# Kernel optimization log

Measured on AMD Instinct MI355X. Metric: run time of the kernel, lower is better.

## Reference

```python
import jax, jax.numpy as jnp
import numpy as np

NUM_EMBEDDINGS = 1024
EMBEDDING_DIM = 256
COMMITMENT_COST = 0.25


def setup_inputs() -> dict:
    key = jax.random.key(0)
    k1, k2 = jax.random.split(key)
    z_e = jax.random.normal(k1, (32, 256, 32, 32), dtype=jnp.float32)
    # nn.init.uniform_(weight, -1/K, 1/K)
    bound = 1.0 / NUM_EMBEDDINGS
    weight = jax.random.uniform(k2, (NUM_EMBEDDINGS, EMBEDDING_DIM), dtype=jnp.float32,
                                minval=-bound, maxval=bound)
    return {"z_e": z_e, "weight": weight}


def reference(z_e, weight):
    B, C, H, W = z_e.shape
    sg = jax.lax.stop_gradient
    # (B, H, W, C) -> (N, C)
    flat = jnp.transpose(z_e, (0, 2, 3, 1)).reshape(-1, C)
    # squared L2 distances to each codebook vector: (N, K)
    dist = (jnp.sum(flat * flat, axis=1, keepdims=True)
            - 2.0 * flat @ weight.T
            + jnp.sum(weight * weight, axis=1))
    indices = jnp.argmin(dist, axis=1)  # (N,)
    # codebook lookup (equivalent to one-hot @ weight)
    quantized = weight[indices].reshape(B, H, W, C)
    quantized = jnp.transpose(quantized, (0, 3, 1, 2))  # (B, C, H, W)
    e_latent = jnp.mean((sg(quantized) - z_e) ** 2)
    q_latent = jnp.mean((quantized - sg(z_e)) ** 2)
    loss = q_latent + COMMITMENT_COST * e_latent
    # straight-through estimator
    quantized_st = z_e + sg(quantized - z_e)
    # codebook usage perplexity: avg_probs = mean of one-hot encodings
    n = flat.shape[0]
    counts = jax.ops.segment_sum(jnp.ones((n,), dtype=z_e.dtype), indices,
                                 num_segments=NUM_EMBEDDINGS)
    avg_probs = counts / n
    perplexity = jnp.exp(-jnp.sum(avg_probs * jnp.log(avg_probs + 1e-10)))
    return (quantized_st, loss, perplexity)
```

## Files before the change

### kernel.cpp

```cpp
#include <hip/hip_runtime.h>
#include <float.h>
#include <math.h>
#include <stdint.h>


#define NB   32
#define NC   256
#define NHW  1024
#define NK   1024
#define NELEM (NB*NC*NHW)
#define GRID_MAIN 512

typedef __attribute__((ext_vector_type(8))) short bf16x8;
typedef __attribute__((ext_vector_type(4))) float f32x4;

__device__ __forceinline__ unsigned short f2bf(float f) {
    unsigned u = __float_as_uint(f);
    u += 0x7FFFu + ((u >> 16) & 1u);
    return (unsigned short)(u >> 16);
}

__global__ __launch_bounds__(256) void vq_prep(const float* __restrict__ w,
                                               float* __restrict__ wsq,
                                               unsigned short* __restrict__ cb,
                                               unsigned int* __restrict__ counts,
                                               unsigned int* __restrict__ lossdone) {
    const int tid = threadIdx.x, b = blockIdx.x;
    const int lane = tid & 63, wv = tid >> 6;
    {
        const int k = b * 4 + wv;
        const float* row = w + k * NC;
        float s = 0.f;
#pragma unroll
        for (int p = 0; p < 4; ++p) { float v = row[lane + p * 64]; s = fmaf(v, v, s); }
#pragma unroll
        for (int off = 32; off; off >>= 1) s += __shfl_down(s, off, 64);
        if (lane == 0) wsq[k] = s;
    }
    const int gt = b * 256 + tid;
    if (gt < 32768) {
        const int t = gt >> 9, p = gt & 511;
        const int cc = p >> 6, l = p & 63;
        const int n = l & 15, quad = l >> 4;
        const float* src = w + (t * 16 + n) * NC + cc * 32 + quad * 8;
        const float4 f0 = *(const float4*)src;
        const float4 f1 = *(const float4*)(src + 4);
        union { unsigned short u[8]; uint4 v; } pk;
        pk.u[0] = f2bf(-2.f * f0.x); pk.u[1] = f2bf(-2.f * f0.y);
        pk.u[2] = f2bf(-2.f * f0.z); pk.u[3] = f2bf(-2.f * f0.w);
        pk.u[4] = f2bf(-2.f * f1.x); pk.u[5] = f2bf(-2.f * f1.y);
        pk.u[6] = f2bf(-2.f * f1.z); pk.u[7] = f2bf(-2.f * f1.w);
        *(uint4*)(cb + (size_t)t * 4096 + cc * 512 + (size_t)l * 8) = pk.v;
    }
    if (b == 128) {
#pragma unroll
        for (int i = 0; i < 4; ++i) counts[tid * 4 + i] = 0u;
        if (tid < 2) lossdone[tid] = 0u;
    }
}

__global__ __launch_bounds__(256) void vq_main3(const float* __restrict__ z,
                                                const float* __restrict__ w,
                                                const float* __restrict__ wsq,
                                                const unsigned short* __restrict__ cb,
                                                unsigned int* __restrict__ counts,
                                                unsigned int* __restrict__ lossdone,
                                                float* __restrict__ out) {
    __shared__ __align__(16) char cbuf[2][32768];
    int*   fidx  = (int*)(cbuf[0]);
    float* pscr  = (float*)(cbuf[0] + 256);
    int*   pidx  = (int*)(cbuf[0] + 768);
    float* lred  = (float*)(cbuf[0] + 1280);
    int*   lflag = (int*)(cbuf[0] + 1296);
    float* red2  = (float*)(cbuf[0] + 1312);

    const int tid  = threadIdx.x;
    const int wv   = tid >> 6, lane = tid & 63;
    const int n    = lane & 15, quad = lane >> 4;
    const int zhalf = wv & 1;
    const int chalf = wv >> 1;
    const int b   = blockIdx.x;
    const int img = b >> 4;
    const int hw0 = (b & 15) << 6;
    const float* zb = z + (size_t)img * (NC * NHW);
    const char* cbb = (const char*)cb;

#define STAGE(ch)                                                              \
    {                                                                          \
        _Pragma("unroll")                                                      \
        for (int i = 0; i < 8; ++i) {                                          \
            const int q = i >> 1, part = i & 1;                                \
            const int tq = (q >> 1) * 32 + (ch) * 2 + (q & 1);                 \
            const char* gsrc = cbb + (size_t)tq * 8192 + part * 4096 + tid * 16;\
            char* ldst = cbuf[(ch) & 1] + i * 4096 + tid * 16;                 \
            __builtin_amdgcn_global_load_lds(                                  \
                (const __attribute__((address_space(1))) unsigned int*)        \
                    (uintptr_t)gsrc,                                           \
                (__attribute__((address_space(3))) unsigned int*)              \
                    (uint32_t)(uintptr_t)ldst,                                 \
                16, 0, 0);                                                     \
        }                                                                      \
    }

    STAGE(0);

    bf16x8 bfr[2][8];
#pragma unroll
    for (int s = 0; s < 2; ++s) {
#pragma unroll
        for (int cc = 0; cc < 8; ++cc) {
            const float* zp = zb + (size_t)(cc * 32 + quad * 8) * NHW
                              + hw0 + zhalf * 32 + s * 16 + n;
            union { unsigned short u[8]; bf16x8 v; } pk;
#pragma unroll
            for (int j = 0; j < 8; ++j) pk.u[j] = f2bf(zp[(size_t)j * NHW]);
            bfr[s][cc] = pk.v;
        }
    }

    float bestv[2] = {FLT_MAX, FLT_MAX};
    int   besti[2] = {0, 0};

    for (int ch = 0; ch < 16; ++ch) {
        __syncthreads();
        if (ch + 1 < 16) STAGE(ch + 1);
        const char* bufc = cbuf[ch & 1];
        const int kt0 = (chalf * 32 + ch * 2) * 16;
        const int kt1 = kt0 + 16;
        const int slot0 = chalf * 2, slot1 = slot0 + 1;
        f32x4 acc00 = *(const f32x4*)(wsq + kt0 + quad * 4);
        f32x4 acc01 = acc00;
        f32x4 acc10 = *(const f32x4*)(wsq + kt1 + quad * 4);
        f32x4 acc11 = acc10;
#pragma unroll
        for (int cc = 0; cc < 8; ++cc) {
            const bf16x8 a0 = *(const bf16x8*)(bufc + slot0 * 8192 + cc * 1024 + lane * 16);
            const bf16x8 a1 = *(const bf16x8*)(bufc + slot1 * 8192 + cc * 1024 + lane * 16);
            acc00 = __builtin_amdgcn_mfma_f32_16x16x32_bf16(a0, bfr[0][cc], acc00, 0, 0, 0);
            acc01 = __builtin_amdgcn_mfma_f32_16x16x32_bf16(a0, bfr[1][cc], acc01, 0, 0, 0);
            acc10 = __builtin_amdgcn_mfma_f32_16x16x32_bf16(a1, bfr[0][cc], acc10, 0, 0, 0);
            acc11 = __builtin_amdgcn_mfma_f32_16x16x32_bf16(a1, bfr[1][cc], acc11, 0, 0, 0);
        }
#pragma unroll
        for (int r = 0; r < 4; ++r) {
            const int k0 = kt0 + quad * 4 + r, k1 = kt1 + quad * 4 + r;
            if (acc00[r] < bestv[0]) { bestv[0] = acc00[r]; besti[0] = k0; }
            if (acc01[r] < bestv[1]) { bestv[1] = acc01[r]; besti[1] = k0; }
            if (acc10[r] < bestv[0]) { bestv[0] = acc10[r]; besti[0] = k1; }
            if (acc11[r] < bestv[1]) { bestv[1] = acc11[r]; besti[1] = k1; }
        }
    }

#pragma unroll
    for (int s = 0; s < 2; ++s) {
        float bv = bestv[s]; int bi = besti[s];
#pragma unroll
        for (int off = 16; off <= 32; off <<= 1) {
            const float ov = __shfl_xor(bv, off, 64);
            const int   ok = __shfl_xor(bi, off, 64);
            if (ov < bv || (ov == bv && ok < bi)) { bv = ov; bi = ok; }
        }
        bestv[s] = bv; besti[s] = bi;
    }
    __syncthreads();
    if (lane < 16) {
#pragma unroll
        for (int s = 0; s < 2; ++s) {
            const int zloc = zhalf * 32 + s * 16 + lane;
            pscr[chalf * 64 + zloc] = bestv[s];
            pidx[chalf * 64 + zloc] = besti[s];
        }
    }
    __syncthreads();
    if (tid < 64) {
        const float s0 = pscr[tid], s1 = pscr[64 + tid];
        const int bi = (s1 < s0) ? pidx[64 + tid] : pidx[tid];
        fidx[tid] = bi;
        atomicAdd(&counts[bi], 1u);
    }
    __syncthreads();

    float lsum = 0.f;
    const int hwl = tid & 63;
    const int cg  = tid >> 6;
    const int myk = fidx[hwl];
    const float* wr  = w + myk * NC;
    const float* zp2 = zb + hw0 + hwl;
    float*       op  = out + (size_t)img * (NC * NHW) + hw0 + hwl;
#pragma unroll 4
    for (int p = 0; p < 16; ++p) {
        const int c0 = cg * 64 + p * 4;
        const float4 q4 = *(const float4*)(wr + c0);
        const float qa[4] = {q4.x, q4.y, q4.z, q4.w};
#pragma unroll
        for (int u = 0; u < 4; ++u) {
            const int c = c0 + u;
            const float zv = zp2[(size_t)c * NHW];
            const float d = qa[u] - zv;
            lsum = fmaf(d, d, lsum);
            op[(size_t)c * NHW] = qa[u];
        }
    }
#pragma unroll
    for (int off = 32; off; off >>= 1) lsum += __shfl_down(lsum, off, 64);
    if (lane == 0) lred[wv] = lsum;
    __syncthreads();
    if (tid == 0) {
        atomicAdd((float*)lossdone, lred[0] + lred[1] + lred[2] + lred[3]);
        const unsigned old = __hip_atomic_fetch_add(&lossdone[1], 1u,
                                 __ATOMIC_ACQ_REL, __HIP_MEMORY_SCOPE_AGENT);
        lflag[0] = (old == GRID_MAIN - 1) ? 1 : 0;
    }
    __syncthreads();
    if (lflag[0]) {
        float s = 0.f;
#pragma unroll
        for (int p = 0; p < 4; ++p) {
            const unsigned c = __hip_atomic_load(&counts[tid + p * 256],
                                   __ATOMIC_RELAXED, __HIP_MEMORY_SCOPE_AGENT);
            const float pr = (float)c * (1.f / 32768.f);
            s = fmaf(pr, logf(pr + 1e-10f), s);
        }
#pragma unroll
        for (int off = 32; off; off >>= 1) s += __shfl_down(s, off, 64);
        if (lane == 0) red2[wv] = s;
        __syncthreads();
        if (tid == 0) {
            const float tot = red2[0] + red2[1] + red2[2] + red2[3];
            const float ls = __hip_atomic_load((float*)lossdone,
                                 __ATOMIC_RELAXED, __HIP_MEMORY_SCOPE_AGENT);
            out[NELEM]     = ls * (1.25f / (float)NELEM);
            out[NELEM + 1] = expf(-tot);
        }
    }
}

extern "C" void kernel_launch(void* const* d_in, const int* in_sizes, int n_in,
                              void* d_out, int out_size, void* d_ws, size_t ws_size,
                              hipStream_t stream) {
    const float* z = (const float*)d_in[0];
    const float* w = (const float*)d_in[1];
    float* out = (float*)d_out;

    float*          wsq      = (float*)d_ws;
    unsigned int*   counts   = (unsigned int*)((char*)d_ws + 4096);
    unsigned int*   lossdone = (unsigned int*)((char*)d_ws + 8192);
    unsigned short* cbfrag   = (unsigned short*)((char*)d_ws + 16384);

    vq_prep <<<256,       256, 0, stream>>>(w, wsq, cbfrag, counts, lossdone);
    vq_main3<<<GRID_MAIN, 256, 0, stream>>>(z, w, wsq, cbfrag, counts, lossdone, out);
}
```

Before: 136.3 us.

## Derive loss from argmin distances and widen blocks to 1024 threads

Blocks grow to 1024 threads covering 128 spatial positions with a 4-way split over the codebook. Each codebook chunk staged in LDS is therefore shared by twice as many positions, and the grid is halved. The loss no longer re-reads z in the output pass. It is rebuilt from the best distance plus a per-position ||z||^2 accumulated while z is loaded. The distance comes from the bf16 MFMA, so the loss may drift slightly from an exact fp32 sum. The output pass now only gathers codebook rows and writes them. The 128 KB LDS footprint allows one block per CU, which may hurt latency hiding.

```diff
diff --git a/kernel.cpp b/kernel.cpp
--- a/kernel.cpp
+++ b/kernel.cpp
@@ -9,7 +9,7 @@
 #define NHW  1024
 #define NK   1024
 #define NELEM (NB*NC*NHW)
-#define GRID_MAIN 512
+#define GRID_MAIN 256
 
 typedef __attribute__((ext_vector_type(8))) short bf16x8;
 typedef __attribute__((ext_vector_type(4))) float f32x4;
@@ -59,40 +59,40 @@
     }
 }
 
-__global__ __launch_bounds__(256) void vq_main3(const float* __restrict__ z,
-                                                const float* __restrict__ w,
-                                                const float* __restrict__ wsq,
-                                                const unsigned short* __restrict__ cb,
-                                                unsigned int* __restrict__ counts,
-                                                unsigned int* __restrict__ lossdone,
-                                                float* __restrict__ out) {
-    __shared__ __align__(16) char cbuf[2][32768];
+__global__ __launch_bounds__(1024, 4) void vq_main4(const float* __restrict__ z,
+                                                    const float* __restrict__ w,
+                                                    const float* __restrict__ wsq,
+                                                    const unsigned short* __restrict__ cb,
+                                                    unsigned int* __restrict__ counts,
+                                                    unsigned int* __restrict__ lossdone,
+                                                    float* __restrict__ out) {
+    __shared__ __align__(16) char cbuf[2][65536];
     int*   fidx  = (int*)(cbuf[0]);
-    float* pscr  = (float*)(cbuf[0] + 256);
-    int*   pidx  = (int*)(cbuf[0] + 768);
-    float* lred  = (float*)(cbuf[0] + 1280);
-    int*   lflag = (int*)(cbuf[0] + 1296);
-    float* red2  = (float*)(cbuf[0] + 1312);
+    float* pscr  = (float*)(cbuf[0] + 512);
+    int*   pidx  = (int*)(cbuf[0] + 2560);
+    float* zsqs  = (float*)(cbuf[0] + 4608);
+    float* lred  = (float*)(cbuf[0] + 5120);
+    int*   lflag = (int*)(cbuf[0] + 5184);
+    float* red2  = (float*)(cbuf[0] + 5200);
 
     const int tid  = threadIdx.x;
     const int wv   = tid >> 6, lane = tid & 63;
     const int n    = lane & 15, quad = lane >> 4;
-    const int zhalf = wv & 1;
-    const int chalf = wv >> 1;
-    const int b   = blockIdx.x;
-    const int img = b >> 4;
-    const int hw0 = (b & 15) << 6;
+    const int zq   = wv & 3;
+    const int cq   = wv >> 2;
+    const int b    = blockIdx.x;
+    const int img  = b >> 3;
+    const int hw0  = (b & 7) << 7;
     const float* zb = z + (size_t)img * (NC * NHW);
     const char* cbb = (const char*)cb;
 
 #define STAGE(ch)                                                              \
     {                                                                          \
         _Pragma("unroll")                                                      \
-        for (int i = 0; i < 8; ++i) {                                          \
-            const int q = i >> 1, part = i & 1;                                \
-            const int tq = (q >> 1) * 32 + (ch) * 2 + (q & 1);                 \
-            const char* gsrc = cbb + (size_t)tq * 8192 + part * 4096 + tid * 16;\
-            char* ldst = cbuf[(ch) & 1] + i * 4096 + tid * 16;                 \
+        for (int i = 0; i < 4; ++i) {                                          \
+            const int t = i * 16 + (ch) * 2 + (tid >> 9);                      \
+            const char* gsrc = cbb + (size_t)t * 8192 + (tid & 511) * 16;      \
+            char* ldst = cbuf[(ch) & 1] + i * 16384 + tid * 16;                \
             __builtin_amdgcn_global_load_lds(                                  \
                 (const __attribute__((address_space(1))) unsigned int*)        \
                     (uintptr_t)gsrc,                                           \
@@ -105,15 +105,20 @@
     STAGE(0);
 
     bf16x8 bfr[2][8];
+    float zsqp[2] = {0.f, 0.f};
 #pragma unroll
     for (int s = 0; s < 2; ++s) {
 #pragma unroll
         for (int cc = 0; cc < 8; ++cc) {
             const float* zp = zb + (size_t)(cc * 32 + quad * 8) * NHW
-                              + hw0 + zhalf * 32 + s * 16 + n;
+                              + hw0 + zq * 32 + s * 16 + n;
             union { unsigned short u[8]; bf16x8 v; } pk;
 #pragma unroll
-            for (int j = 0; j < 8; ++j) pk.u[j] = f2bf(zp[(size_t)j * NHW]);
+            for (int j = 0; j < 8; ++j) {
+                const float f = zp[(size_t)j * NHW];
+                zsqp[s] = fmaf(f, f, zsqp[s]);
+                pk.u[j] = f2bf(f);
+            }
             bfr[s][cc] = pk.v;
         }
     }
@@ -121,21 +126,21 @@
     float bestv[2] = {FLT_MAX, FLT_MAX};
     int   besti[2] = {0, 0};
 
-    for (int ch = 0; ch < 16; ++ch) {
+    for (int ch = 0; ch < 8; ++ch) {
         __syncthreads();
-        if (ch + 1 < 16) STAGE(ch + 1);
+        if (ch + 1 < 8) STAGE(ch + 1);
         const char* bufc = cbuf[ch & 1];
-        const int kt0 = (chalf * 32 + ch * 2) * 16;
+        const int kt0 = (cq * 16 + ch * 2) * 16;
         const int kt1 = kt0 + 16;
-        const int slot0 = chalf * 2, slot1 = slot0 + 1;
+        const int so0 = (cq * 2) * 8192, so1 = so0 + 8192;
         f32x4 acc00 = *(const f32x4*)(wsq + kt0 + quad * 4);
         f32x4 acc01 = acc00;
         f32x4 acc10 = *(const f32x4*)(wsq + kt1 + quad * 4);
         f32x4 acc11 = acc10;
 #pragma unroll
         for (int cc = 0; cc < 8; ++cc) {
-            const bf16x8 a0 = *(const bf16x8*)(bufc + slot0 * 8192 + cc * 1024 + lane * 16);
-            const bf16x8 a1 = *(const bf16x8*)(bufc + slot1 * 8192 + cc * 1024 + lane * 16);
+            const bf16x8 a0 = *(const bf16x8*)(bufc + so0 + cc * 1024 + lane * 16);
+            const bf16x8 a1 = *(const bf16x8*)(bufc + so1 + cc * 1024 + lane * 16);
             acc00 = __builtin_amdgcn_mfma_f32_16x16x32_bf16(a0, bfr[0][cc], acc00, 0, 0, 0);
             acc01 = __builtin_amdgcn_mfma_f32_16x16x32_bf16(a0, bfr[1][cc], acc01, 0, 0, 0);
             acc10 = __builtin_amdgcn_mfma_f32_16x16x32_bf16(a1, bfr[0][cc], acc10, 0, 0, 0);
@@ -153,77 +158,79 @@
 
 #pragma unroll
     for (int s = 0; s < 2; ++s) {
-        float bv = bestv[s]; int bi = besti[s];
+        float bv = bestv[s]; int bi = besti[s]; float zs = zsqp[s];
 #pragma unroll
         for (int off = 16; off <= 32; off <<= 1) {
             const float ov = __shfl_xor(bv, off, 64);
             const int   ok = __shfl_xor(bi, off, 64);
             if (ov < bv || (ov == bv && ok < bi)) { bv = ov; bi = ok; }
-        }
-        bestv[s] = bv; besti[s] = bi;
+            zs += __shfl_xor(zs, off, 64);
+        }
+        bestv[s] = bv; besti[s] = bi; zsqp[s] = zs;
     }
     __syncthreads();
     if (lane < 16) {
 #pragma unroll
         for (int s = 0; s < 2; ++s) {
-            const int zloc = zhalf * 32 + s * 16 + lane;
-            pscr[chalf * 64 + zloc] = bestv[s];
-            pidx[chalf * 64 + zloc] = besti[s];
-        }
-    }
-    __syncthreads();
-    if (tid < 64) {
-        const float s0 = pscr[tid], s1 = pscr[64 + tid];
-        const int bi = (s1 < s0) ? pidx[64 + tid] : pidx[tid];
+            const int zloc = zq * 32 + s * 16 + lane;
+            pscr[cq * 128 + zloc] = bestv[s];
+            pidx[cq * 128 + zloc] = besti[s];
+            if (cq == 0) zsqs[zloc] = zsqp[s];
+        }
+    }
+    __syncthreads();
+    if (tid < 128) {
+        float bv = pscr[tid]; int bi = pidx[tid];
+#pragma unroll
+        for (int q = 1; q < 4; ++q) {
+            const float v = pscr[q * 128 + tid];
+            if (v < bv) { bv = v; bi = pidx[q * 128 + tid]; }
+        }
         fidx[tid] = bi;
         atomicAdd(&counts[bi], 1u);
-    }
-    __syncthreads();
-
-    float lsum = 0.f;
-    const int hwl = tid & 63;
-    const int cg  = tid >> 6;
-    const int myk = fidx[hwl];
-    const float* wr  = w + myk * NC;
-    const float* zp2 = zb + hw0 + hwl;
-    float*       op  = out + (size_t)img * (NC * NHW) + hw0 + hwl;
-#pragma unroll 4
-    for (int p = 0; p < 16; ++p) {
-        const int c0 = cg * 64 + p * 4;
-        const float4 q4 = *(const float4*)(wr + c0);
-        const float qa[4] = {q4.x, q4.y, q4.z, q4.w};
-#pragma unroll
-        for (int u = 0; u < 4; ++u) {
-            const int c = c0 + u;
-            const float zv = zp2[(size_t)c * NHW];
-            const float d = qa[u] - zv;
-            lsum = fmaf(d, d, lsum);
-            op[(size_t)c * NHW] = qa[u];
-        }
-    }
-#pragma unroll
-    for (int off = 32; off; off >>= 1) lsum += __shfl_down(lsum, off, 64);
-    if (lane == 0) lred[wv] = lsum;
+        float ln = bv + zsqs[tid];
+#pragma unroll
+        for (int off = 32; off; off >>= 1) ln += __shfl_down(ln, off, 64);
+        if ((tid & 63) == 0) lred[tid >> 6] = ln;
+    }
     __syncthreads();
     if (tid == 0) {
-        atomicAdd((float*)lossdone, lred[0] + lred[1] + lred[2] + lred[3]);
+        atomicAdd((float*)lossdone, lred[0] + lred[1]);
         const unsigned old = __hip_atomic_fetch_add(&lossdone[1], 1u,
                                  __ATOMIC_ACQ_REL, __HIP_MEMORY_SCOPE_AGENT);
         lflag[0] = (old == GRID_MAIN - 1) ? 1 : 0;
     }
+
+    {
+        const int hwl = tid & 127;
+        const int cg  = tid >> 7;
+        const int myk = fidx[hwl];
+        const float* wr = w + myk * NC + cg * 32;
+        float* ob = out + (size_t)img * (NC * NHW) + (size_t)(cg * 32) * NHW + hw0 + hwl;
+#pragma unroll
+        for (int p = 0; p < 8; ++p) {
+            const float4 q4 = *(const float4*)(wr + p * 4);
+            ob[(size_t)(p * 4 + 0) * NHW] = q4.x;
+            ob[(size_t)(p * 4 + 1) * NHW] = q4.y;
+            ob[(size_t)(p * 4 + 2) * NHW] = q4.z;
+            ob[(size_t)(p * 4 + 3) * NHW] = q4.w;
+        }
+    }
     __syncthreads();
     if (lflag[0]) {
-        float s = 0.f;
-#pragma unroll
-        for (int p = 0; p < 4; ++p) {
-            const unsigned c = __hip_atomic_load(&counts[tid + p * 256],
-                                   __ATOMIC_RELAXED, __HIP_MEMORY_SCOPE_AGENT);
-            const float pr = (float)c * (1.f / 32768.f);
-            s = fmaf(pr, logf(pr + 1e-10f), s);
-        }
-#pragma unroll
-        for (int off = 32; off; off >>= 1) s += __shfl_down(s, off, 64);
-        if (lane == 0) red2[wv] = s;
+        if (tid < 256) {
+            float s = 0.f;
+#pragma unroll
+            for (int p = 0; p < 4; ++p) {
+                const unsigned c = __hip_atomic_load(&counts[tid + p * 256],
+                                       __ATOMIC_RELAXED, __HIP_MEMORY_SCOPE_AGENT);
+                const float pr = (float)c * (1.f / 32768.f);
+                s = fmaf(pr, logf(pr + 1e-10f), s);
+            }
+#pragma unroll
+            for (int off = 32; off; off >>= 1) s += __shfl_down(s, off, 64);
+            if (lane == 0) red2[tid >> 6] = s;
+        }
         __syncthreads();
         if (tid == 0) {
             const float tot = red2[0] + red2[1] + red2[2] + red2[3];
@@ -247,6 +254,6 @@
     unsigned int*   lossdone = (unsigned int*)((char*)d_ws + 8192);
     unsigned short* cbfrag   = (unsigned short*)((char*)d_ws + 16384);
 
-    vq_prep <<<256,       256, 0, stream>>>(w, wsq, cbfrag, counts, lossdone);
-    vq_main3<<<GRID_MAIN, 256, 0, stream>>>(z, w, wsq, cbfrag, counts, lossdone, out);
-}
+    vq_prep <<<256,       256,  0, stream>>>(w, wsq, cbfrag, counts, lossdone);
+    vq_main4<<<GRID_MAIN, 1024, 0, stream>>>(z, w, wsq, cbfrag, counts, lossdone, out);
+}
```

After: 149.4 us. +9.7%, slower.
